# Kernel optimization log

Hardware: AMD Instinct MI355X
Metric: run time of the kernel (lower is better)

## Reference

```python
import jax, jax.numpy as jnp
import numpy as np

EPS = 1e-5

def _face_normals(v, vi):
    # v: [B,V,3], vi: [F,3] -> [B,F,3]
    pts = v[:, vi]                                  # [B,F,3,3]
    n = jnp.cross(pts[:, :, 1] - pts[:, :, 0], pts[:, :, 2] - pts[:, :, 0])
    norm = jnp.linalg.norm(n, axis=-1, keepdims=True)
    return n / jnp.where(norm < EPS, 1.0, norm)

def _vert_normals(v, vi):
    fn = _face_normals(v, vi)                       # [B,F,3]
    fn_rep = jnp.repeat(fn, 3, axis=1)              # [B,3F,3] (one copy per face vertex)
    vn = jnp.zeros_like(v).at[:, vi.reshape(-1)].add(fn_rep)
    norm = jnp.linalg.norm(vn, axis=-1, keepdims=True)
    return vn / jnp.where(norm < EPS, 1.0, norm)

def _values_to_uv(values, index_image, bary_image):
    # values: [B,V,C]; index_image/bary_image: [U,U,3] -> [B,C,U,U]
    mask = jnp.all(index_image != -1, axis=-1)      # [U,U]
    idx = jnp.clip(index_image, 0, values.shape[1] - 1)
    vals = values[:, idx]                           # [B,U,U,3,C]
    uv = jnp.einsum('buvkc,uvk->bcuv', vals, bary_image.astype(values.dtype))
    return uv * mask[None, None].astype(values.dtype)

def _grid_sample_bilinear(img, gx, gy):
    # img: [B,C,H,W]; gx,gy: [N] in [-1,1]; align_corners=False, zero padding
    B, C, H, W = img.shape
    ix = ((gx + 1.0) * W - 1.0) * 0.5
    iy = ((gy + 1.0) * H - 1.0) * 0.5
    x0 = jnp.floor(ix); y0 = jnp.floor(iy)
    x1 = x0 + 1.0;      y1 = y0 + 1.0
    wx1 = ix - x0; wx0 = 1.0 - wx1
    wy1 = iy - y0; wy0 = 1.0 - wy1
    def gather(xi, yi):
        valid = (xi >= 0) & (xi < W) & (yi >= 0) & (yi < H)
        xc = jnp.clip(xi, 0, W - 1).astype(jnp.int32)
        yc = jnp.clip(yi, 0, H - 1).astype(jnp.int32)
        return img[:, :, yc, xc] * valid.astype(img.dtype)  # [B,C,N]
    return (gather(x0, y0) * (wx0 * wy0) + gather(x1, y0) * (wx1 * wy0)
          + gather(x0, y1) * (wx0 * wy1) + gather(x1, y1) * (wx1 * wy1))

def _sample_uv(values_uv, uv_coords, v2uv):
    g = uv_coords * 2.0 - 1.0                       # [T,2]
    vals = _grid_sample_bilinear(values_uv, g[:, 0], g[:, 1])  # [B,C,T]
    vals = jnp.transpose(vals, (0, 2, 1))           # [B,T,C]
    return vals[:, v2uv].mean(axis=2)               # [B,V,C]

def setup_inputs() -> dict:
    key = jax.random.key(0)
    ks = jax.random.split(key, 6)
    B, V, Fc, U, T, K = 8, 100000, 200000, 1024, 110000, 2
    verts = jax.random.normal(ks[0], (B, V, 3), jnp.float32)
    vi = jax.random.randint(ks[1], (Fc, 3), 0, V, dtype=jnp.int32)
    index_image = jax.random.randint(ks[2], (U, U, 3), 0, V, dtype=jnp.int32)
    bary_image = jax.random.uniform(ks[3], (U, U, 3), jnp.float32)
    vt = jax.random.uniform(ks[4], (T, 2), jnp.float32)
    v2uv = jax.random.randint(ks[5], (V, K), 0, T, dtype=jnp.int32)
    return {"verts": verts, "bary_image": bary_image, "vt": vt,
            "vi": vi, "index_image": index_image, "v2uv": v2uv}

def reference(verts, bary_image, vt, vi, index_image, v2uv):
    vn = _vert_normals(verts, vi)                   # [B,V,3]
    uv = _values_to_uv(vn, index_image, bary_image) # [B,3,U,U]
    return _sample_uv(uv, vt, v2uv)                 # [B,V,3]
```

## Files before the change

kernel.cpp:

```cpp
#include <hip/hip_runtime.h>
#include <hip/hip_fp16.h>

#define EPS 1e-5f

constexpr int B = 8;
constexpr int V = 100000;
constexpr int F = 200000;
constexpr int U = 1024;
constexpr int T = 110000;
constexpr int CAP = 24;

constexpr int NBUK = (V + 127) / 128;
constexpr int N4   = (3 * F) / 4;
constexpr int EB   = (N4 + 255) / 256;
constexpr int TRB  = (V + 255) / 256;

constexpr int FQ   = 2;
constexpr int FNB  = (F * 8 / FQ + 255) / 256;
constexpr int TQ   = 2;
constexpr int CPB  = (T / TQ + 255) / 256;
constexpr int SQ   = 1;
constexpr int VQ   = 2;

struct alignas(8) h4 { __half2 a, b; };
__device__ inline h4 pack_h4(float x, float y, float z) {
    h4 r; r.a = __floats2half2_rn(x, y); r.b = __floats2half2_rn(z, 0.0f);
    return r;
}
__device__ inline float3 unpack_h4(h4 v) {
    float2 xy = __half22float2(v.a);
    float2 zw = __half22float2(v.b);
    return make_float3(xy.x, xy.y, zw.x);
}

struct alignas(16) Corner16 { unsigned lo, hi; __half2 w01; __half2 w2_; };
__device__ inline Corner16 pack_corner(int i0, int i1, int i2,
                                       float w0, float w1, float w2) {
    unsigned long long x = (unsigned long long)(unsigned)i0
                         | ((unsigned long long)(unsigned)i1 << 21)
                         | ((unsigned long long)(unsigned)i2 << 42);
    Corner16 c;
    c.lo = (unsigned)x;
    c.hi = (unsigned)(x >> 32);
    c.w01 = __floats2half2_rn(w0, w1);
    c.w2_ = __floats2half2_rn(w2, 0.0f);
    return c;
}

__global__ void k1_pre(const float* __restrict__ verts,
                       float4* __restrict__ vertsT,
                       const int* __restrict__ vi,
                       int* __restrict__ hist) {
    __shared__ int lh[NBUK];
    int blk = blockIdx.x;
    if (blk < TRB) {
        int v = blk * 256 + threadIdx.x;
        if (v >= V) return;
        float4 row[8];
#pragma unroll
        for (int b = 0; b < 8; ++b) {
            const float* p = verts + (size_t)b * V * 3 + (size_t)v * 3;
            row[b] = make_float4(p[0], p[1], p[2], 0.0f);
        }
        float4* dst = vertsT + (size_t)v * 8;
#pragma unroll
        for (int b = 0; b < 8; ++b) dst[b] = row[b];
    } else {
        int k = blk - TRB;
        for (int i = threadIdx.x; i < NBUK; i += 256) lh[i] = 0;
        __syncthreads();
        int m4 = k * 256 + threadIdx.x;
        if (m4 < N4) {
            int4 e = ((const int4*)vi)[m4];
            atomicAdd(&lh[e.x >> 7], 1);
            atomicAdd(&lh[e.y >> 7], 1);
            atomicAdd(&lh[e.z >> 7], 1);
            atomicAdd(&lh[e.w >> 7], 1);
        }
        __syncthreads();
        for (int b = threadIdx.x; b < NBUK; b += 256) hist[k * NBUK + b] = lh[b];
    }
}

__global__ void k2_fused(const int* __restrict__ vi,
                         const float4* __restrict__ vertsT,
                         h4* __restrict__ fn,
                         const int* __restrict__ index_image,
                         const float* __restrict__ bary_image,
                         const float* __restrict__ vt,
                         Corner16* __restrict__ corners,
                         int* __restrict__ hist,
                         int* __restrict__ tot) {
    int blk = blockIdx.x;

    if (blk < FNB) {
        int id = blk * 256 + threadIdx.x;
        if (id >= F * 8 / FQ) return;
        int b = id & 7;
        int fbase = id >> 3;

        int ia[FQ], ib[FQ], ic[FQ];
        float4 p0[FQ], p1[FQ], p2[FQ];
#pragma unroll
        for (int q = 0; q < FQ; ++q) {
            int f = fbase + q * (F / FQ);
            ia[q] = vi[f * 3 + 0];
            ib[q] = vi[f * 3 + 1];
            ic[q] = vi[f * 3 + 2];
        }
#pragma unroll
        for (int q = 0; q < FQ; ++q) {
            p0[q] = vertsT[(size_t)ia[q] * 8 + b];
            p1[q] = vertsT[(size_t)ib[q] * 8 + b];
            p2[q] = vertsT[(size_t)ic[q] * 8 + b];
        }
#pragma unroll
        for (int q = 0; q < FQ; ++q) {
            int f = fbase + q * (F / FQ);
            float e1x = p1[q].x - p0[q].x, e1y = p1[q].y - p0[q].y, e1z = p1[q].z - p0[q].z;
            float e2x = p2[q].x - p0[q].x, e2y = p2[q].y - p0[q].y, e2z = p2[q].z - p0[q].z;

            float nx = e1y * e2z - e1z * e2y;
            float ny = e1z * e2x - e1x * e2z;
            float nz = e1x * e2y - e1y * e2x;

            float norm = sqrtf(nx * nx + ny * ny + nz * nz);
            float inv = (norm < EPS) ? 1.0f : (1.0f / norm);
            fn[(size_t)f * 8 + b] = pack_h4(nx * inv, ny * inv, nz * inv);
        }
        return;
    }

    if (blk < FNB + CPB) {
        int tbase = (blk - FNB) * 256 + threadIdx.x;
        if (tbase >= T / TQ) return;
#pragma unroll
        for (int qq = 0; qq < TQ; ++qq) {
            int t = tbase + qq * (T / TQ);

            float gx = vt[t * 2 + 0];
            float gy = vt[t * 2 + 1];
            float ix = gx * (float)U - 0.5f;
            float iy = gy * (float)U - 0.5f;

            float x0f = floorf(ix);
            float y0f = floorf(iy);
            int x0 = (int)x0f;
            int y0 = (int)y0f;
            float wx1 = ix - x0f, wx0 = 1.0f - wx1;
            float wy1 = iy - y0f, wy0 = 1.0f - wy1;

#pragma unroll
            for (int c = 0; c < 4; ++c) {
                int cy = c >> 1, cx = c & 1;
                int y = y0 + cy;
                int x = x0 + cx;
                int i0 = 0, i1 = 0, i2 = 0;
                float w0 = 0.0f, w1 = 0.0f, w2 = 0.0f;
                if (x >= 0 && x < U && y >= 0 && y < U) {
                    float w = (cy ? wy1 : wy0) * (cx ? wx1 : wx0);
                    int pix = y * U + x;
                    int j0 = index_image[pix * 3 + 0];
                    int j1 = index_image[pix * 3 + 1];
                    int j2 = index_image[pix * 3 + 2];
                    float m = (j0 != -1 && j1 != -1 && j2 != -1) ? 1.0f : 0.0f;
                    float wm = w * m;
                    i0 = min(max(j0, 0), V - 1);
                    i1 = min(max(j1, 0), V - 1);
                    i2 = min(max(j2, 0), V - 1);
                    w0 = wm * bary_image[pix * 3 + 0];
                    w1 = wm * bary_image[pix * 3 + 1];
                    w2 = wm * bary_image[pix * 3 + 2];
                }
                corners[t * 4 + c] = pack_corner(i0, i1, i2, w0, w1, w2);
            }
        }
        return;
    }

    {
        __shared__ int part[256];
        int b = blk - FNB - CPB;
        int th = threadIdx.x;
        int k0 = th * 3;
        int c0 = (k0     < EB) ? hist[(k0    ) * NBUK + b] : 0;
        int c1 = (k0 + 1 < EB) ? hist[(k0 + 1) * NBUK + b] : 0;
        int c2 = (k0 + 2 < EB) ? hist[(k0 + 2) * NBUK + b] : 0;
        int local = c0 + c1 + c2;
        part[th] = local;
        __syncthreads();
        for (int off = 1; off < 256; off <<= 1) {
            int x = (th >= off) ? part[th - off] : 0;
            __syncthreads();
            part[th] += x;
            __syncthreads();
        }
        int excl = part[th] - local;
        if (th == 255) tot[b] = part[255];
        if (k0     < EB) hist[(k0    ) * NBUK + b] = excl;
        if (k0 + 1 < EB) hist[(k0 + 1) * NBUK + b] = excl + c0;
        if (k0 + 2 < EB) hist[(k0 + 2) * NBUK + b] = excl + c0 + c1;
    }
}

template <int NT>
__device__ inline void scan_base(const int* __restrict__ tot,
                                 int* pre, int* part) {
    constexpr int CH = (NBUK + NT - 1) / NT;
    int th = threadIdx.x;
    int loc[CH];
    int local = 0;
#pragma unroll
    for (int j = 0; j < CH; ++j) {
        int idx = th * CH + j;
        int c = (idx < NBUK) ? tot[idx] : 0;
        loc[j] = local;
        local += c;
    }
    part[th] = local;
    __syncthreads();
    for (int off = 1; off < NT; off <<= 1) {
        int x = (th >= off) ? part[th - off] : 0;
        __syncthreads();
        part[th] += x;
        __syncthreads();
    }
    int excl = part[th] - local;
#pragma unroll
    for (int j = 0; j < CH; ++j) {
        int idx = th * CH + j;
        if (idx < NBUK) pre[idx] = excl + loc[j];
    }
    if (th == NT - 1) pre[NBUK] = part[NT - 1];
    __syncthreads();
}

__global__ void k4_scatter(const int* __restrict__ vi,
                           const int* __restrict__ off,
                           const int* __restrict__ tot,
                           int* __restrict__ pairs) {
    __shared__ int lh[NBUK];
    __shared__ int pre[NBUK + 1];
    __shared__ int part[256];
    scan_base<256>(tot, pre, part);

    int k = blockIdx.x;
    for (int i = threadIdx.x; i < NBUK; i += 256) lh[i] = 0;
    __syncthreads();
    int m4 = k * 256 + threadIdx.x;
    if (m4 >= N4) return;
    int4 e = ((const int4*)vi)[m4];
    int be = m4 * 4;
    int vv[4] = {e.x, e.y, e.z, e.w};
#pragma unroll
    for (int j = 0; j < 4; ++j) {
        int v = vv[j];
        int b = v >> 7;
        int r = atomicAdd(&lh[b], 1);
        int pos = pre[b] + off[k * NBUK + b] + r;
        pairs[pos] = ((v & 127) << 18) | ((be + j) / 3);
    }
}

__global__ __launch_bounds__(512) void k5_gather(
        const int* __restrict__ pairs,
        const int* __restrict__ tot,
        const h4* __restrict__ fn,
        h4* __restrict__ vn) {
    __shared__ int cnt[128];
    __shared__ int rows[128 * CAP];
    __shared__ int pre[NBUK + 1];
    __shared__ int part[512];
    scan_base<512>(tot, pre, part);

    int tid = threadIdx.x;
    if (tid < 128) cnt[tid] = 0;
    __syncthreads();

    int b = blockIdx.x;
    int start = pre[b], end = pre[b + 1];
    for (int i = start + tid; i < end; i += 512) {
        int pk = pairs[i];
        int vl = pk >> 18;
        int f = pk & 0x3FFFF;
        int pos = atomicAdd(&cnt[vl], 1);
        if (pos < CAP) rows[vl * CAP + pos] = f;
    }
    __syncthreads();

    int v0 = b << 7;
    for (int id = tid; id < 128 * 8; id += 512) {
        int vl = id >> 3, b8 = id & 7;
        int v = v0 + vl;
        if (v >= V) continue;
        int deg = min(cnt[vl], CAP);
        float ax = 0.0f, ay = 0.0f, az = 0.0f;
        int j = 0;
        for (; j + 1 < deg; j += 2) {
            h4 r0 = fn[(size_t)rows[vl * CAP + j] * 8 + b8];
            h4 r1 = fn[(size_t)rows[vl * CAP + j + 1] * 8 + b8];
            float3 n0 = unpack_h4(r0);
            float3 n1 = unpack_h4(r1);
            ax += n0.x + n1.x; ay += n0.y + n1.y; az += n0.z + n1.z;
        }
        if (j < deg) {
            float3 n = unpack_h4(fn[(size_t)rows[vl * CAP + j] * 8 + b8]);
            ax += n.x; ay += n.y; az += n.z;
        }
        float nn = sqrtf(ax * ax + ay * ay + az * az);
        float inv = (nn < EPS) ? 1.0f : (1.0f / nn);
        vn[(size_t)v * 8 + b8] = pack_h4(ax * inv, ay * inv, az * inv);
    }
}

__global__ void sample_points(const h4* __restrict__ vn,
                              const Corner16* __restrict__ corners,
                              h4* __restrict__ vals) {
    int id = blockIdx.x * blockDim.x + threadIdx.x;
    if (id >= T * 8) return;
    int b = id & 7;
    int t = id >> 3;

    float ax = 0.0f, ay = 0.0f, az = 0.0f;
    Corner16 cr[4];
#pragma unroll
    for (int c = 0; c < 4; ++c) cr[c] = corners[t * 4 + c];
    h4 q[12];
#pragma unroll
    for (int c = 0; c < 4; ++c) {
        unsigned long long x = (unsigned long long)cr[c].lo
                             | ((unsigned long long)cr[c].hi << 32);
        int i0 = (int)(x & 0x1FFFFF);
        int i1 = (int)((x >> 21) & 0x1FFFFF);
        int i2 = (int)(x >> 42);
        q[c * 3 + 0] = vn[(size_t)i0 * 8 + b];
        q[c * 3 + 1] = vn[(size_t)i1 * 8 + b];
        q[c * 3 + 2] = vn[(size_t)i2 * 8 + b];
    }
#pragma unroll
    for (int c = 0; c < 4; ++c) {
        float2 w01 = __half22float2(cr[c].w01);
        float w2 = __low2float(cr[c].w2_);
        float3 q0 = unpack_h4(q[c * 3 + 0]);
        float3 q1 = unpack_h4(q[c * 3 + 1]);
        float3 q2 = unpack_h4(q[c * 3 + 2]);
        ax += w01.x * q0.x + w01.y * q1.x + w2 * q2.x;
        ay += w01.x * q0.y + w01.y * q1.y + w2 * q2.y;
        az += w01.x * q0.z + w01.y * q1.z + w2 * q2.z;
    }
    vals[(size_t)t * 8 + b] = pack_h4(ax, ay, az);
}

__global__ void gather_out(const h4* __restrict__ vals,
                           const int* __restrict__ v2uv,
                           float* __restrict__ out) {
    int id = blockIdx.x * blockDim.x + threadIdx.x;
    if (id >= (V / VQ) * 8) return;
    int b = id & 7;
    int vb = id >> 3;

    int t0[VQ], t1[VQ];
    h4 xa[VQ], ya[VQ];
#pragma unroll
    for (int s = 0; s < VQ; ++s) {
        int v = vb + s * (V / VQ);
        t0[s] = v2uv[v * 2 + 0];
        t1[s] = v2uv[v * 2 + 1];
    }
#pragma unroll
    for (int s = 0; s < VQ; ++s) {
        xa[s] = vals[(size_t)t0[s] * 8 + b];
        ya[s] = vals[(size_t)t1[s] * 8 + b];
    }
#pragma unroll
    for (int s = 0; s < VQ; ++s) {
        int v = vb + s * (V / VQ);
        float3 x = unpack_h4(xa[s]);
        float3 y = unpack_h4(ya[s]);
        float* o = out + (size_t)b * V * 3 + (size_t)v * 3;
        o[0] = 0.5f * (x.x + y.x);
        o[1] = 0.5f * (x.y + y.y);
        o[2] = 0.5f * (x.z + y.z);
    }
}

extern "C" void kernel_launch(void* const* d_in, const int* in_sizes, int n_in,
                              void* d_out, int out_size, void* d_ws, size_t ws_size,
                              hipStream_t stream) {
    const float* verts   = (const float*)d_in[0];
    const float* bary    = (const float*)d_in[1];
    const float* vt      = (const float*)d_in[2];
    const int*   vi      = (const int*)d_in[3];
    const int*   idx_img = (const int*)d_in[4];
    const int*   v2uv    = (const int*)d_in[5];
    float* out = (float*)d_out;

    float4*   vertsT  = (float4*)d_ws;
    h4*       vn      = (h4*)d_ws;
    h4*       fn      = (h4*)(vertsT + (size_t)V * 8);
    h4*       vals    = fn;
    Corner16* corners = (Corner16*)((char*)fn + (size_t)F * 8 * sizeof(h4));
    int*      hist    = (int*)(corners + (size_t)T * 4);
    int*      tot     = hist + (size_t)EB * NBUK;
    int*      pairs   = tot + NBUK;

    const int BLK = 256;
    k1_pre<<<TRB + EB, BLK, 0, stream>>>(verts, vertsT, vi, hist);
    k2_fused<<<FNB + CPB + NBUK, BLK, 0, stream>>>(
        vi, vertsT, fn, idx_img, bary, vt, corners, hist, tot);
    k4_scatter<<<EB, BLK, 0, stream>>>(vi, hist, tot, pairs);
    k5_gather<<<NBUK, 512, 0, stream>>>(pairs, tot, fn, vn);
    sample_points<<<(T * 8 + BLK - 1) / BLK, BLK, 0, stream>>>(
        vn, corners, vals);
    gather_out<<<((V / VQ) * 8 + BLK - 1) / BLK, BLK, 0, stream>>>(
        vals, v2uv, out);
}
```

Baseline: 177.1 us.

## Compute face normals directly from batch-major verts and transpose normals afterward

Removes the vertex transpose pass from k1 and has the face-normal stage gather directly from the original [B,V,3] vertex layout, one batch per block group, writing batch-major face normals. A new block range in k4_scatter then transposes the face normals into the face-major [F,8] layout that k5_gather expects. This drops the 25.6 MB vertsT write and re-read, at the cost of uncoalesced 12-byte gathers from the original layout and an extra transpose of the half-precision normals.

```diff
diff --git a/kernel.cpp b/kernel.cpp
--- a/kernel.cpp
+++ b/kernel.cpp
@@ -13,13 +13,11 @@
 constexpr int NBUK = (V + 127) / 128;
 constexpr int N4   = (3 * F) / 4;
 constexpr int EB   = (N4 + 255) / 256;
-constexpr int TRB  = (V + 255) / 256;
-
-constexpr int FQ   = 2;
-constexpr int FNB  = (F * 8 / FQ + 255) / 256;
+
+constexpr int FCH  = (F + 255) / 256;
+constexpr int FNB2 = FCH * 8;
 constexpr int TQ   = 2;
 constexpr int CPB  = (T / TQ + 255) / 256;
-constexpr int SQ   = 1;
 constexpr int VQ   = 2;
 
 struct alignas(8) h4 { __half2 a, b; };
@@ -47,44 +45,27 @@
     return c;
 }
 
-__global__ void k1_pre(const float* __restrict__ verts,
-                       float4* __restrict__ vertsT,
-                       const int* __restrict__ vi,
+__global__ void k1_pre(const int* __restrict__ vi,
                        int* __restrict__ hist) {
     __shared__ int lh[NBUK];
-    int blk = blockIdx.x;
-    if (blk < TRB) {
-        int v = blk * 256 + threadIdx.x;
-        if (v >= V) return;
-        float4 row[8];
-#pragma unroll
-        for (int b = 0; b < 8; ++b) {
-            const float* p = verts + (size_t)b * V * 3 + (size_t)v * 3;
-            row[b] = make_float4(p[0], p[1], p[2], 0.0f);
-        }
-        float4* dst = vertsT + (size_t)v * 8;
-#pragma unroll
-        for (int b = 0; b < 8; ++b) dst[b] = row[b];
-    } else {
-        int k = blk - TRB;
-        for (int i = threadIdx.x; i < NBUK; i += 256) lh[i] = 0;
-        __syncthreads();
-        int m4 = k * 256 + threadIdx.x;
-        if (m4 < N4) {
-            int4 e = ((const int4*)vi)[m4];
-            atomicAdd(&lh[e.x >> 7], 1);
-            atomicAdd(&lh[e.y >> 7], 1);
-            atomicAdd(&lh[e.z >> 7], 1);
-            atomicAdd(&lh[e.w >> 7], 1);
-        }
-        __syncthreads();
-        for (int b = threadIdx.x; b < NBUK; b += 256) hist[k * NBUK + b] = lh[b];
-    }
+    int k = blockIdx.x;
+    for (int i = threadIdx.x; i < NBUK; i += 256) lh[i] = 0;
+    __syncthreads();
+    int m4 = k * 256 + threadIdx.x;
+    if (m4 < N4) {
+        int4 e = ((const int4*)vi)[m4];
+        atomicAdd(&lh[e.x >> 7], 1);
+        atomicAdd(&lh[e.y >> 7], 1);
+        atomicAdd(&lh[e.z >> 7], 1);
+        atomicAdd(&lh[e.w >> 7], 1);
+    }
+    __syncthreads();
+    for (int b = threadIdx.x; b < NBUK; b += 256) hist[k * NBUK + b] = lh[b];
 }
 
 __global__ void k2_fused(const int* __restrict__ vi,
-                         const float4* __restrict__ vertsT,
-                         h4* __restrict__ fn,
+                         const float* __restrict__ verts,
+                         h4* __restrict__ fnT,
                          const int* __restrict__ index_image,
                          const float* __restrict__ bary_image,
                          const float* __restrict__ vt,
@@ -93,46 +74,37 @@
                          int* __restrict__ tot) {
     int blk = blockIdx.x;
 
-    if (blk < FNB) {
-        int id = blk * 256 + threadIdx.x;
-        if (id >= F * 8 / FQ) return;
-        int b = id & 7;
-        int fbase = id >> 3;
-
-        int ia[FQ], ib[FQ], ic[FQ];
-        float4 p0[FQ], p1[FQ], p2[FQ];
-#pragma unroll
-        for (int q = 0; q < FQ; ++q) {
-            int f = fbase + q * (F / FQ);
-            ia[q] = vi[f * 3 + 0];
-            ib[q] = vi[f * 3 + 1];
-            ic[q] = vi[f * 3 + 2];
-        }
-#pragma unroll
-        for (int q = 0; q < FQ; ++q) {
-            p0[q] = vertsT[(size_t)ia[q] * 8 + b];
-            p1[q] = vertsT[(size_t)ib[q] * 8 + b];
-            p2[q] = vertsT[(size_t)ic[q] * 8 + b];
-        }
-#pragma unroll
-        for (int q = 0; q < FQ; ++q) {
-            int f = fbase + q * (F / FQ);
-            float e1x = p1[q].x - p0[q].x, e1y = p1[q].y - p0[q].y, e1z = p1[q].z - p0[q].z;
-            float e2x = p2[q].x - p0[q].x, e2y = p2[q].y - p0[q].y, e2z = p2[q].z - p0[q].z;
-
-            float nx = e1y * e2z - e1z * e2y;
-            float ny = e1z * e2x - e1x * e2z;
-            float nz = e1x * e2y - e1y * e2x;
-
-            float norm = sqrtf(nx * nx + ny * ny + nz * nz);
-            float inv = (norm < EPS) ? 1.0f : (1.0f / norm);
-            fn[(size_t)f * 8 + b] = pack_h4(nx * inv, ny * inv, nz * inv);
-        }
+    if (blk < FNB2) {
+        int b = blk & 7;
+        int f = (blk >> 3) * 256 + threadIdx.x;
+        if (f >= F) return;
+
+        const float* vb = verts + (size_t)b * V * 3;
+        int i0 = vi[f * 3 + 0];
+        int i1 = vi[f * 3 + 1];
+        int i2 = vi[f * 3 + 2];
+        const float* q0 = vb + (size_t)i0 * 3;
+        const float* q1 = vb + (size_t)i1 * 3;
+        const float* q2 = vb + (size_t)i2 * 3;
+        float p0x = q0[0], p0y = q0[1], p0z = q0[2];
+        float p1x = q1[0], p1y = q1[1], p1z = q1[2];
+        float p2x = q2[0], p2y = q2[1], p2z = q2[2];
+
+        float e1x = p1x - p0x, e1y = p1y - p0y, e1z = p1z - p0z;
+        float e2x = p2x - p0x, e2y = p2y - p0y, e2z = p2z - p0z;
+
+        float nx = e1y * e2z - e1z * e2y;
+        float ny = e1z * e2x - e1x * e2z;
+        float nz = e1x * e2y - e1y * e2x;
+
+        float norm = sqrtf(nx * nx + ny * ny + nz * nz);
+        float inv = (norm < EPS) ? 1.0f : (1.0f / norm);
+        fnT[(size_t)b * F + f] = pack_h4(nx * inv, ny * inv, nz * inv);
         return;
     }
 
-    if (blk < FNB + CPB) {
-        int tbase = (blk - FNB) * 256 + threadIdx.x;
+    if (blk < FNB2 + CPB) {
+        int tbase = (blk - FNB2) * 256 + threadIdx.x;
         if (tbase >= T / TQ) return;
 #pragma unroll
         for (int qq = 0; qq < TQ; ++qq) {
@@ -180,7 +152,7 @@
 
     {
         __shared__ int part[256];
-        int b = blk - FNB - CPB;
+        int b = blk - FNB2 - CPB;
         int th = threadIdx.x;
         int k0 = th * 3;
         int c0 = (k0     < EB) ? hist[(k0    ) * NBUK + b] : 0;
@@ -238,13 +210,29 @@
 __global__ void k4_scatter(const int* __restrict__ vi,
                            const int* __restrict__ off,
                            const int* __restrict__ tot,
-                           int* __restrict__ pairs) {
+                           int* __restrict__ pairs,
+                           const h4* __restrict__ fnT,
+                           h4* __restrict__ fn) {
+    int blk = blockIdx.x;
+    if (blk >= EB) {
+        int f = (blk - EB) * 256 + threadIdx.x;
+        if (f >= F) return;
+        h4 row[8];
+#pragma unroll
+        for (int b = 0; b < 8; ++b) row[b] = fnT[(size_t)b * F + f];
+        float4* dst = (float4*)(fn + (size_t)f * 8);
+        const float4* src = (const float4*)row;
+#pragma unroll
+        for (int i = 0; i < 4; ++i) dst[i] = src[i];
+        return;
+    }
+
     __shared__ int lh[NBUK];
     __shared__ int pre[NBUK + 1];
     __shared__ int part[256];
     scan_base<256>(tot, pre, part);
 
-    int k = blockIdx.x;
+    int k = blk;
     for (int i = threadIdx.x; i < NBUK; i += 256) lh[i] = 0;
     __syncthreads();
     int m4 = k * 256 + threadIdx.x;
@@ -395,9 +383,9 @@
     const int*   v2uv    = (const int*)d_in[5];
     float* out = (float*)d_out;
 
-    float4*   vertsT  = (float4*)d_ws;
+    h4*       fnT     = (h4*)d_ws;
     h4*       vn      = (h4*)d_ws;
-    h4*       fn      = (h4*)(vertsT + (size_t)V * 8);
+    h4*       fn      = (h4*)((char*)d_ws + (size_t)F * 8 * sizeof(h4));
     h4*       vals    = fn;
     Corner16* corners = (Corner16*)((char*)fn + (size_t)F * 8 * sizeof(h4));
     int*      hist    = (int*)(corners + (size_t)T * 4);
@@ -405,10 +393,10 @@
     int*      pairs   = tot + NBUK;
 
     const int BLK = 256;
-    k1_pre<<<TRB + EB, BLK, 0, stream>>>(verts, vertsT, vi, hist);
-    k2_fused<<<FNB + CPB + NBUK, BLK, 0, stream>>>(
-        vi, vertsT, fn, idx_img, bary, vt, corners, hist, tot);
-    k4_scatter<<<EB, BLK, 0, stream>>>(vi, hist, tot, pairs);
+    k1_pre<<<EB, BLK, 0, stream>>>(vi, hist);
+    k2_fused<<<FNB2 + CPB + NBUK, BLK, 0, stream>>>(
+        vi, verts, fnT, idx_img, bary, vt, corners, hist, tot);
+    k4_scatter<<<EB + FCH, BLK, 0, stream>>>(vi, hist, tot, pairs, fnT, fn);
     k5_gather<<<NBUK, 512, 0, stream>>>(pairs, tot, fn, vn);
     sample_points<<<(T * 8 + BLK - 1) / BLK, BLK, 0, stream>>>(
         vn, corners, vals);
```

Result: slower. 190.4 us (+7.5%).
